# Kernel tuning notes

Measured on AMD Instinct MI355X. Metric: run time of the kernel, lower is better.

Reference implementation:

```python
import jax, jax.numpy as jnp
import numpy as np


def squash(t, axis=-1):
    # scale = |t|^2/(1+|t|^2) ; out = scale * t/|t|  (matches torch version incl. no eps)
    sn = jnp.sum(t * t, axis=axis, keepdims=True)
    return sn / (1.0 + sn) * t / jnp.sqrt(sn)


def setup_inputs() -> dict:
    key = jax.random.key(0)
    ks = jax.random.split(key, 6)
    B = 512
    return {
        "x": jax.random.normal(ks[0], (B, 1, 28, 28), jnp.float32),
        "conv_w": jax.random.normal(ks[1], (256, 1, 9, 9), jnp.float32) * 0.05,
        "conv_b": jax.random.normal(ks[2], (256,), jnp.float32) * 0.05,
        # 8 primary-capsule convs Conv2d(256,32,9,9,stride=2) stacked on output channels
        "prim_w": jax.random.normal(ks[3], (8 * 32, 256, 9, 9), jnp.float32) * 0.02,
        "prim_b": jax.random.normal(ks[4], (8 * 32,), jnp.float32) * 0.02,
        # route_weights: (num_capsules=10, num_route_nodes=1152, input_dim=8, output_dim=16)
        "route_w": jax.random.normal(ks[5], (10, 1152, 8, 16), jnp.float32),
    }


def reference(x, conv_w, conv_b, prim_w, prim_b, route_w):
    B = x.shape[0]
    dn = ("NCHW", "OIHW", "NCHW")
    # stem: 1->256, k9 s1, no activation in original code
    y = jax.lax.conv_general_dilated(x, conv_w, (1, 1), "VALID", dimension_numbers=dn)
    y = y + conv_b[None, :, None, None]                      # [B,256,20,20]
    # primary caps: 8 parallel convs 256->32, k9 s2, fused into one conv
    p = jax.lax.conv_general_dilated(y, prim_w, (2, 2), "VALID", dimension_numbers=dn)
    p = p + prim_b[None, :, None, None]                      # [B,256,6,6]
    p = p.reshape(B, 8, 32 * 6 * 6)                          # per-capsule flatten (C,H,W)
    u = squash(jnp.transpose(p, (0, 2, 1)))                  # [B,1152,8]
    # priors[b,c,r,o] = u[b,r,:] @ route_w[c,r,:,:]
    priors = jnp.einsum("bri,crio->bcro", u, route_w)        # [B,10,1152,16]
    blog = jnp.zeros((B, 10, 1152), priors.dtype)
    v = None
    for _ in range(3):  # num_iterations = 3 (fixed)
        probs = jax.nn.softmax(blog, axis=2)[..., None]      # softmax over route dim
        v = squash(jnp.sum(priors * probs, axis=2, keepdims=True))  # [B,10,1,16]
        blog = blog + jnp.sum(priors * v, axis=-1)           # agreement update
    v = v[:, :, 0, :]                                        # [B,10,16]
    logits = jnp.sqrt(jnp.sum(v * v, axis=-1))               # capsule lengths
    return jax.nn.softmax(logits, axis=-1)                   # [B,10]
```

## Files before the change

kernel.cpp:

```cpp
#include <hip/hip_runtime.h>
#include <cstddef>
#include <cstdint>

typedef _Float16 f16;
typedef _Float16 f16x4 __attribute__((ext_vector_type(4)));
typedef _Float16 f16x8 __attribute__((ext_vector_type(8)));
typedef float f32x4 __attribute__((ext_vector_type(4)));
typedef float f32x16 __attribute__((ext_vector_type(16)));

#define AS1 __attribute__((address_space(1)))
#define AS3 __attribute__((address_space(3)))


__device__ __forceinline__ float wave_max(float v) {
#pragma unroll
  for (int m = 1; m < 64; m <<= 1) v = fmaxf(v, __shfl_xor(v, m, 64));
  return v;
}
__device__ __forceinline__ float wave_sum(float v) {
#pragma unroll
  for (int m = 1; m < 64; m <<= 1) v += __shfl_xor(v, m, 64);
  return v;
}

__global__ __launch_bounds__(256) void conv1_kernel(
    const float* __restrict__ x, const float* __restrict__ w,
    const float* __restrict__ bias, f16* __restrict__ y16) {
  const int b   = blockIdx.x;
  const int oc0 = blockIdx.y * 64;
  const int t   = threadIdx.x;
  const int tx  = t & 15;
  const int ty  = t >> 4;
  const int oxg = ty & 3;
  const int oy0 = ty >> 2;

  __shared__ float x_s[784];
  __shared__ float w_s[81][68];

  for (int idx = t; idx < 784; idx += 256) x_s[idx] = x[b * 784 + idx];
  for (int idx = t; idx < 64 * 81; idx += 256) {
    const int oc_l = idx / 81, k = idx % 81;
    w_s[k][oc_l] = w[(oc0 + oc_l) * 81 + k];
  }
  __syncthreads();

  float bz[4];
#pragma unroll
  for (int j = 0; j < 4; ++j) bz[j] = bias[oc0 + tx * 4 + j];

  for (int m = 0; m < 5; ++m) {
    const int oy = oy0 + m * 4;
    float acc[4][5];
#pragma unroll
    for (int j = 0; j < 4; ++j)
#pragma unroll
      for (int pp = 0; pp < 5; ++pp) acc[j][pp] = 0.f;

#pragma unroll
    for (int ky = 0; ky < 9; ++ky) {
      float xv[13];
      const int base = (oy + ky) * 28 + oxg * 5;
#pragma unroll
      for (int jj = 0; jj < 13; ++jj) xv[jj] = x_s[base + jj];
#pragma unroll
      for (int kx = 0; kx < 9; ++kx) {
        const float4 w4 = *reinterpret_cast<const float4*>(&w_s[ky * 9 + kx][tx * 4]);
#pragma unroll
        for (int pp = 0; pp < 5; ++pp) {
          const float xval = xv[kx + pp];
          acc[0][pp] += w4.x * xval;
          acc[1][pp] += w4.y * xval;
          acc[2][pp] += w4.z * xval;
          acc[3][pp] += w4.w * xval;
        }
      }
    }
#pragma unroll
    for (int pp = 0; pp < 5; ++pp) {
      f16x4 st;
#pragma unroll
      for (int j = 0; j < 4; ++j) st[j] = (f16)(acc[j][pp] + bz[j]);
      const int px = oy * 20 + oxg * 5 + pp;
      *(f16x4*)&y16[((size_t)b * 400 + px) * 256 + oc0 + tx * 4] = st;
    }
  }
}

__global__ __launch_bounds__(256) void wprep_kernel(const float* __restrict__ w,
                                                    f16* __restrict__ w16) {
  const int idx = blockIdx.x * 256 + threadIdx.x;
  const int kk  = idx >> 13;
  const int rem = idx & 8191;
  const int oc  = rem >> 5;
  const int icg = rem & 31;
  f16x8 v;
#pragma unroll
  for (int j = 0; j < 8; ++j)
    v[j] = (f16)w[((size_t)(oc * 256 + icg * 8 + j)) * 81 + kk];
  *(f16x8*)&w16[((size_t)kk * 256 + oc) * 256 + icg * 8] = v;
}

__global__ __launch_bounds__(256, 3) void conv2_mfma(
    const f16* __restrict__ y16, const f16* __restrict__ w16,
    float* __restrict__ p4) {
  const int h       = blockIdx.x;
  const int ntile   = h % 144;
  const int variant = h / 144;
  const int octile  = variant >> 2;
  const int ks      = variant & 3;
  const int oc0     = octile * 64;
  const int cicb    = ks * 64;

  const int tid  = threadIdx.x;
  const int lane = tid & 63;
  const int wave = tid >> 6;
  const int l31  = lane & 31;
  const int hi   = lane >> 5;
  const int wm   = wave >> 1;
  const int wn   = wave & 1;

  __shared__ char smem[49152];

  const int lr   = lane >> 3;
  const int swz  = ((lane & 7) ^ (lr & 7)) * 8;
  const f16* aPtr[2];
  uint32_t aLoff[2];
#pragma unroll
  for (int q = 0; q < 2; ++q) {
    const int g = wave * 2 + q;
    const int oc = oc0 + g * 8 + lr;
    aPtr[q]  = w16 + (size_t)oc * 256 + cicb + swz;
    aLoff[q] = (uint32_t)__builtin_amdgcn_readfirstlane(g * 1024);
  }
  const f16* bPtr[4];
  uint32_t bLoff[4];
#pragma unroll
  for (int q = 0; q < 4; ++q) {
    const int g   = wave * 4 + q;
    const int n   = ntile * 128 + g * 8 + lr;
    const int b   = n / 36;
    const int op  = n - b * 36;
    const int oy  = op / 6;
    const int ox  = op - oy * 6;
    bPtr[q]  = y16 + ((size_t)b * 400 + 40 * oy + 2 * ox) * 256 + cicb + swz;
    bLoff[q] = (uint32_t)__builtin_amdgcn_readfirstlane(8192 + g * 1024);
  }

  f32x16 acc0 = {0.f}, acc1 = {0.f};
#pragma unroll
  for (int r = 0; r < 16; ++r) { acc0[r] = 0.f; acc1[r] = 0.f; }

  auto stage = [&](int bb, int kkn) {
    const int ky    = kkn / 9;
    const int kx    = kkn - ky * 9;
    const int koffB = (20 * ky + kx) * 256;
    const int koffA = kkn * 65536;
#pragma unroll
    for (int q = 0; q < 2; ++q)
      __builtin_amdgcn_global_load_lds(
          (const AS1 uint32_t*)(aPtr[q] + koffA),
          (AS3 uint32_t*)((AS3 char*)smem + bb + aLoff[q]), 16, 0, 0);
#pragma unroll
    for (int q = 0; q < 4; ++q)
      __builtin_amdgcn_global_load_lds(
          (const AS1 uint32_t*)(bPtr[q] + koffB),
          (AS3 uint32_t*)((AS3 char*)smem + bb + bLoff[q]), 16, 0, 0);
  };

  const int rowA  = (wm * 32 + l31) * 128;
  const int rowB  = 8192 + (wn * 64 + l31) * 128;
  const int sbase = l31 & 7;

  stage(0, 0);

  for (int kk = 0; kk < 81; ++kk) {
    const int cur = (kk & 1) * 24576;
    if (kk < 80) {
      stage(cur ^ 24576, kk + 1);
      asm volatile("s_waitcnt vmcnt(6)" ::: "memory");
    } else {
      asm volatile("s_waitcnt vmcnt(0)" ::: "memory");
    }
    __builtin_amdgcn_s_barrier();

    const char* bufp = smem + cur;
#pragma unroll
    for (int kc = 0; kc < 4; ++kc) {
      const int sw = (((kc * 2 + hi) ^ sbase) << 4);
      const f16x8 av = *(const f16x8*)(bufp + rowA + sw);
      const f16x8 b0 = *(const f16x8*)(bufp + rowB + sw);
      const f16x8 b1 = *(const f16x8*)(bufp + rowB + 32 * 128 + sw);
      acc0 = __builtin_amdgcn_mfma_f32_32x32x16_f16(av, b0, acc0, 0, 0, 0);
      acc1 = __builtin_amdgcn_mfma_f32_32x32x16_f16(av, b1, acc1, 0, 0, 0);
    }
    __builtin_amdgcn_s_barrier();
  }

  float* pk = p4 + (size_t)ks * 4718592;
#pragma unroll
  for (int nf = 0; nf < 2; ++nf) {
    const int n  = ntile * 128 + wn * 64 + nf * 32 + l31;
    const int b  = n / 36;
    const int op = n - b * 36;
    float* pb = pk + (size_t)b * 9216 + op;
    const f32x16 a = nf ? acc1 : acc0;
#pragma unroll
    for (int r = 0; r < 16; ++r) {
      const int oc = oc0 + wm * 32 + (r & 3) + 8 * (r >> 2) + 4 * hi;
      pb[oc * 36] = a[r];
    }
  }
}

__global__ __launch_bounds__(256) void squash_kernel(const float* __restrict__ p4,
                                                     const float* __restrict__ bias,
                                                     float* __restrict__ u) {
  const int idx = blockIdx.x * 256 + threadIdx.x;
  if (idx >= 512 * 1152) return;
  const int b = idx / 1152;
  const int r = idx % 1152;
  const int c2 = r / 36;
  const int s  = r % 36;
  const size_t base = (size_t)b * 9216 + c2 * 36 + s;
  float tv[8];
  float sn = 0.f;
#pragma unroll
  for (int g = 0; g < 8; ++g) {
    const size_t off = base + (size_t)g * 32 * 36;
    float t = p4[off] + p4[off + 4718592] + p4[off + 2 * 4718592] +
              p4[off + 3 * 4718592] + bias[g * 32 + c2];
    tv[g] = t;
    sn += t * t;
  }
  const float scale = sn / ((1.f + sn) * sqrtf(sn));
  float* up = u + (size_t)idx * 8;
#pragma unroll
  for (int g = 0; g < 8; ++g) up[g] = tv[g] * scale;
}

__global__ __launch_bounds__(256) void routing_kernel(const float* __restrict__ u,
                                                      const float* __restrict__ rw,
                                                      float* __restrict__ logits) {
  const int b    = blockIdx.x;
  const int c    = blockIdx.y;
  const int t    = threadIdx.x;
  const int og   = t & 3;
  const int rg   = t >> 2;
  const int lane = t & 63;
  const int wid  = t >> 6;

  __shared__ float u_s[1152 * 9];
  __shared__ float blog_s[1152];
  __shared__ float red[8];
  __shared__ float sred[64];

  for (int idx = t; idx < 1152 * 8; idx += 256)
    u_s[(idx >> 3) * 9 + (idx & 7)] = u[(size_t)b * 9216 + idx];
  for (int idx = t; idx < 1152; idx += 256) blog_s[idx] = 0.f;
  __syncthreads();

  float pr[18][4];
  const float* rwc = rw + (size_t)c * 1152 * 128;
#pragma unroll
  for (int k = 0; k < 18; ++k) {
    const int r = rg + 64 * k;
    float a0 = 0.f, a1 = 0.f, a2 = 0.f, a3 = 0.f;
#pragma unroll
    for (int i = 0; i < 8; ++i) {
      const float uv = u_s[r * 9 + i];
      const float4 w4 = *reinterpret_cast<const float4*>(rwc + (size_t)r * 128 + i * 16 + og * 4);
      a0 += uv * w4.x; a1 += uv * w4.y; a2 += uv * w4.z; a3 += uv * w4.w;
    }
    pr[k][0] = a0; pr[k][1] = a1; pr[k][2] = a2; pr[k][3] = a3;
  }

  float sn = 0.f;
  float vj[4] = {0.f, 0.f, 0.f, 0.f};

  for (int it = 0; it < 3; ++it) {
    float lmax = -3.4e38f;
    for (int idx = t; idx < 1152; idx += 256) lmax = fmaxf(lmax, blog_s[idx]);
    lmax = wave_max(lmax);
    if (lane == 0) red[wid] = lmax;
    __syncthreads();
    const float gmax = fmaxf(fmaxf(red[0], red[1]), fmaxf(red[2], red[3]));
    float lsum = 0.f;
    for (int idx = t; idx < 1152; idx += 256) lsum += expf(blog_s[idx] - gmax);
    lsum = wave_sum(lsum);
    if (lane == 0) red[4 + wid] = lsum;
    __syncthreads();
    const float ginv = 1.f / (red[4] + red[5] + red[6] + red[7]);

    float sp0 = 0.f, sp1 = 0.f, sp2 = 0.f, sp3 = 0.f;
#pragma unroll
    for (int k = 0; k < 18; ++k) {
      const int r = rg + 64 * k;
      const float pb = expf(blog_s[r] - gmax) * ginv;
      sp0 += pr[k][0] * pb; sp1 += pr[k][1] * pb;
      sp2 += pr[k][2] * pb; sp3 += pr[k][3] * pb;
    }
#pragma unroll
    for (int m = 4; m < 64; m <<= 1) {
      sp0 += __shfl_xor(sp0, m, 64);
      sp1 += __shfl_xor(sp1, m, 64);
      sp2 += __shfl_xor(sp2, m, 64);
      sp3 += __shfl_xor(sp3, m, 64);
    }
    if (lane < 4) {
      sred[wid * 16 + lane * 4 + 0] = sp0;
      sred[wid * 16 + lane * 4 + 1] = sp1;
      sred[wid * 16 + lane * 4 + 2] = sp2;
      sred[wid * 16 + lane * 4 + 3] = sp3;
    }
    __syncthreads();

    sn = 0.f;
#pragma unroll
    for (int o = 0; o < 16; ++o) {
      const float sv = sred[o] + sred[16 + o] + sred[32 + o] + sred[48 + o];
      sn += sv * sv;
    }
    const float scale = sn / ((1.f + sn) * sqrtf(sn));
#pragma unroll
    for (int j = 0; j < 4; ++j) {
      const int o = og * 4 + j;
      vj[j] = (sred[o] + sred[16 + o] + sred[32 + o] + sred[48 + o]) * scale;
    }

    if (it < 2) {
#pragma unroll
      for (int k = 0; k < 18; ++k) {
        float bp = pr[k][0] * vj[0] + pr[k][1] * vj[1] + pr[k][2] * vj[2] + pr[k][3] * vj[3];
        bp += __shfl_xor(bp, 1, 64);
        bp += __shfl_xor(bp, 2, 64);
        if (og == 0) blog_s[rg + 64 * k] += bp;
      }
      __syncthreads();
    }
  }
  if (t == 0) logits[b * 10 + c] = sn / (1.f + sn);
}

__global__ __launch_bounds__(256) void out_softmax_kernel(const float* __restrict__ logits,
                                                          float* __restrict__ out) {
  const int b = blockIdx.x * 256 + threadIdx.x;
  if (b >= 512) return;
  float l[10];
  float mx = -3.4e38f;
#pragma unroll
  for (int cc = 0; cc < 10; ++cc) {
    l[cc] = logits[b * 10 + cc];
    mx = fmaxf(mx, l[cc]);
  }
  float s = 0.f;
#pragma unroll
  for (int cc = 0; cc < 10; ++cc) {
    l[cc] = expf(l[cc] - mx);
    s += l[cc];
  }
  const float inv = 1.f / s;
#pragma unroll
  for (int cc = 0; cc < 10; ++cc) out[b * 10 + cc] = l[cc] * inv;
}

extern "C" void kernel_launch(void* const* d_in, const int* in_sizes, int n_in,
                              void* d_out, int out_size, void* d_ws, size_t ws_size,
                              hipStream_t stream) {
  const float* x       = (const float*)d_in[0];
  const float* conv_w  = (const float*)d_in[1];
  const float* conv_b  = (const float*)d_in[2];
  const float* prim_w  = (const float*)d_in[3];
  const float* prim_b  = (const float*)d_in[4];
  const float* route_w = (const float*)d_in[5];
  float* out = (float*)d_out;

  f16* y16      = (f16*)d_ws;
  f16* w16      = y16 + 52428800;
  float* p4     = (float*)(w16 + 5308416);
  float* u      = p4 + 4 * 4718592;
  float* logits = u + 4718592;

  conv1_kernel<<<dim3(512, 4), 256, 0, stream>>>(x, conv_w, conv_b, y16);
  wprep_kernel<<<2592, 256, 0, stream>>>(prim_w, w16);
  conv2_mfma<<<2304, 256, 0, stream>>>(y16, w16, p4);
  squash_kernel<<<(512 * 1152 + 255) / 256, 256, 0, stream>>>(p4, prim_b, u);
  routing_kernel<<<dim3(512, 10), 256, 0, stream>>>(u, route_w, logits);
  out_softmax_kernel<<<2, 256, 0, stream>>>(logits, out);
}
```

Measured before the change: 734.0 us.

## Enlarge conv2 MFMA block tile to 128x128 with 2x2 fragments per wave

The primary-capsule conv GEMM block tile grows from 64 output channels to 128. Each wave now computes a 64x64 region using four 32x32 MFMA accumulators instead of two, which halves the grid and doubles operand reuse from LDS and global loads. It also raises wave priority around the MFMA section. In exchange it uses more LDS (64KB) and more registers, lowering occupancy to 2 blocks per CU, and the grid of 1152 blocks gives fewer blocks per CU to hide latency.

```diff
diff --git a/kernel.cpp b/kernel.cpp
--- a/kernel.cpp
+++ b/kernel.cpp
@@ -100,15 +100,15 @@
   *(f16x8*)&w16[((size_t)kk * 256 + oc) * 256 + icg * 8] = v;
 }
 
-__global__ __launch_bounds__(256, 3) void conv2_mfma(
+__global__ __launch_bounds__(256, 2) void conv2_mfma(
     const f16* __restrict__ y16, const f16* __restrict__ w16,
     float* __restrict__ p4) {
   const int h       = blockIdx.x;
   const int ntile   = h % 144;
   const int variant = h / 144;
-  const int octile  = variant >> 2;
+  const int mtile   = variant >> 2;
   const int ks      = variant & 3;
-  const int oc0     = octile * 64;
+  const int oc0     = mtile * 128;
   const int cicb    = ks * 64;
 
   const int tid  = threadIdx.x;
@@ -119,15 +119,15 @@
   const int wm   = wave >> 1;
   const int wn   = wave & 1;
 
-  __shared__ char smem[49152];
+  __shared__ char smem[65536];
 
   const int lr   = lane >> 3;
   const int swz  = ((lane & 7) ^ (lr & 7)) * 8;
-  const f16* aPtr[2];
-  uint32_t aLoff[2];
-#pragma unroll
-  for (int q = 0; q < 2; ++q) {
-    const int g = wave * 2 + q;
+  const f16* aPtr[4];
+  uint32_t aLoff[4];
+#pragma unroll
+  for (int q = 0; q < 4; ++q) {
+    const int g  = wave * 4 + q;
     const int oc = oc0 + g * 8 + lr;
     aPtr[q]  = w16 + (size_t)oc * 256 + cicb + swz;
     aLoff[q] = (uint32_t)__builtin_amdgcn_readfirstlane(g * 1024);
@@ -136,27 +136,29 @@
   uint32_t bLoff[4];
 #pragma unroll
   for (int q = 0; q < 4; ++q) {
-    const int g   = wave * 4 + q;
-    const int n   = ntile * 128 + g * 8 + lr;
-    const int b   = n / 36;
-    const int op  = n - b * 36;
-    const int oy  = op / 6;
-    const int ox  = op - oy * 6;
+    const int g  = wave * 4 + q;
+    const int n  = ntile * 128 + g * 8 + lr;
+    const int b  = n / 36;
+    const int op = n - b * 36;
+    const int oy = op / 6;
+    const int ox = op - oy * 6;
     bPtr[q]  = y16 + ((size_t)b * 400 + 40 * oy + 2 * ox) * 256 + cicb + swz;
-    bLoff[q] = (uint32_t)__builtin_amdgcn_readfirstlane(8192 + g * 1024);
-  }
-
-  f32x16 acc0 = {0.f}, acc1 = {0.f};
-#pragma unroll
-  for (int r = 0; r < 16; ++r) { acc0[r] = 0.f; acc1[r] = 0.f; }
+    bLoff[q] = (uint32_t)__builtin_amdgcn_readfirstlane(16384 + g * 1024);
+  }
+
+  f32x16 acc00, acc01, acc10, acc11;
+#pragma unroll
+  for (int r = 0; r < 16; ++r) {
+    acc00[r] = 0.f; acc01[r] = 0.f; acc10[r] = 0.f; acc11[r] = 0.f;
+  }
 
   auto stage = [&](int bb, int kkn) {
     const int ky    = kkn / 9;
     const int kx    = kkn - ky * 9;
     const int koffB = (20 * ky + kx) * 256;
-    const int koffA = kkn * 65536;
-#pragma unroll
-    for (int q = 0; q < 2; ++q)
+    const size_t koffA = (size_t)kkn * 65536;
+#pragma unroll
+    for (int q = 0; q < 4; ++q)
       __builtin_amdgcn_global_load_lds(
           (const AS1 uint32_t*)(aPtr[q] + koffA),
           (AS3 uint32_t*)((AS3 char*)smem + bb + aLoff[q]), 16, 0, 0);
@@ -167,47 +169,56 @@
           (AS3 uint32_t*)((AS3 char*)smem + bb + bLoff[q]), 16, 0, 0);
   };
 
-  const int rowA  = (wm * 32 + l31) * 128;
-  const int rowB  = 8192 + (wn * 64 + l31) * 128;
+  const int rowA  = (wm * 64 + l31) * 128;
+  const int rowB  = 16384 + (wn * 64 + l31) * 128;
   const int sbase = l31 & 7;
 
   stage(0, 0);
 
   for (int kk = 0; kk < 81; ++kk) {
-    const int cur = (kk & 1) * 24576;
+    const int cur = (kk & 1) * 32768;
     if (kk < 80) {
-      stage(cur ^ 24576, kk + 1);
-      asm volatile("s_waitcnt vmcnt(6)" ::: "memory");
+      stage(cur ^ 32768, kk + 1);
+      asm volatile("s_waitcnt vmcnt(8)" ::: "memory");
     } else {
       asm volatile("s_waitcnt vmcnt(0)" ::: "memory");
     }
     __builtin_amdgcn_s_barrier();
 
     const char* bufp = smem + cur;
+    __builtin_amdgcn_s_setprio(1);
 #pragma unroll
     for (int kc = 0; kc < 4; ++kc) {
       const int sw = (((kc * 2 + hi) ^ sbase) << 4);
-      const f16x8 av = *(const f16x8*)(bufp + rowA + sw);
+      const f16x8 a0 = *(const f16x8*)(bufp + rowA + sw);
+      const f16x8 a1 = *(const f16x8*)(bufp + rowA + 32 * 128 + sw);
       const f16x8 b0 = *(const f16x8*)(bufp + rowB + sw);
       const f16x8 b1 = *(const f16x8*)(bufp + rowB + 32 * 128 + sw);
-      acc0 = __builtin_amdgcn_mfma_f32_32x32x16_f16(av, b0, acc0, 0, 0, 0);
-      acc1 = __builtin_amdgcn_mfma_f32_32x32x16_f16(av, b1, acc1, 0, 0, 0);
-    }
+      acc00 = __builtin_amdgcn_mfma_f32_32x32x16_f16(a0, b0, acc00, 0, 0, 0);
+      acc01 = __builtin_amdgcn_mfma_f32_32x32x16_f16(a0, b1, acc01, 0, 0, 0);
+      acc10 = __builtin_amdgcn_mfma_f32_32x32x16_f16(a1, b0, acc10, 0, 0, 0);
+      acc11 = __builtin_amdgcn_mfma_f32_32x32x16_f16(a1, b1, acc11, 0, 0, 0);
+    }
+    __builtin_amdgcn_s_setprio(0);
     __builtin_amdgcn_s_barrier();
   }
 
   float* pk = p4 + (size_t)ks * 4718592;
 #pragma unroll
-  for (int nf = 0; nf < 2; ++nf) {
-    const int n  = ntile * 128 + wn * 64 + nf * 32 + l31;
-    const int b  = n / 36;
-    const int op = n - b * 36;
-    float* pb = pk + (size_t)b * 9216 + op;
-    const f32x16 a = nf ? acc1 : acc0;
-#pragma unroll
-    for (int r = 0; r < 16; ++r) {
-      const int oc = oc0 + wm * 32 + (r & 3) + 8 * (r >> 2) + 4 * hi;
-      pb[oc * 36] = a[r];
+  for (int af = 0; af < 2; ++af) {
+#pragma unroll
+    for (int bf = 0; bf < 2; ++bf) {
+      const f32x16 a = af ? (bf ? acc11 : acc10) : (bf ? acc01 : acc00);
+      const int n  = ntile * 128 + wn * 64 + bf * 32 + l31;
+      const int b  = n / 36;
+      const int op = n - b * 36;
+      float* pb = pk + (size_t)b * 9216 + op;
+      const int ocb = oc0 + wm * 64 + af * 32 + 4 * hi;
+#pragma unroll
+      for (int r = 0; r < 16; ++r) {
+        const int oc = ocb + (r & 3) + 8 * (r >> 2);
+        pb[oc * 36] = a[r];
+      }
     }
   }
 }
@@ -382,7 +393,7 @@
 
   conv1_kernel<<<dim3(512, 4), 256, 0, stream>>>(x, conv_w, conv_b, y16);
   wprep_kernel<<<2592, 256, 0, stream>>>(prim_w, w16);
-  conv2_mfma<<<2304, 256, 0, stream>>>(y16, w16, p4);
+  conv2_mfma<<<1152, 256, 0, stream>>>(y16, w16, p4);
   squash_kernel<<<(512 * 1152 + 255) / 256, 256, 0, stream>>>(p4, prim_b, u);
   routing_kernel<<<dim3(512, 10), 256, 0, stream>>>(u, route_w, logits);
   out_softmax_kernel<<<2, 256, 0, stream>>>(logits, out);
```

Measured after the change: 682.8 us. 7.0% less time.
